# Kernel tuning notes

Hardware: AMD Instinct MI355X
Metric: run time of the kernel (lower is better)

## Reference

```python
import jax, jax.numpy as jnp
import numpy as np

STROKE_SIZE = 200000
WORD_SIZE = 100000
EMB_DIM = 128
BATCH = 16384
MAX_STROKE_LEN = 20
N_SAMPLE = 5


def setup_inputs() -> dict:
    key = jax.random.key(0)
    k1, k2, k3, k4, k5 = jax.random.split(key, 5)
    initrange = 0.5 / EMB_DIM
    u_emb = jax.random.uniform(k1, (STROKE_SIZE, EMB_DIM), jnp.float32,
                               minval=-initrange, maxval=initrange)
    # original inits v to zeros (degenerate loss); use small random values so
    # the score/loss path is numerically non-trivial for kernel testing.
    v_emb = jax.random.normal(k2, (WORD_SIZE, EMB_DIM), jnp.float32) * initrange
    pos_u = jax.random.randint(k3, (BATCH, MAX_STROKE_LEN), 0, STROKE_SIZE)
    pos_v = jax.random.randint(k4, (BATCH, MAX_STROKE_LEN), 0, WORD_SIZE)
    neg_v = jax.random.randint(k5, (BATCH, N_SAMPLE, MAX_STROKE_LEN), 0, WORD_SIZE)
    return {
        "max_stroke_len": MAX_STROKE_LEN,
        "n_sample": N_SAMPLE,
        "pos_u": pos_u,
        "pos_v": pos_v,
        "neg_v": neg_v,
        "u_emb": u_emb,
        "v_emb": v_emb,
    }


def reference(max_stroke_len, n_sample, pos_u, pos_v, neg_v, u_emb, v_emb):
    # gather + mean-pool n-gram embeddings: [B, L, D] -> [B, D]
    emb_u = u_emb[pos_u].mean(axis=1)
    emb_v = v_emb[pos_v].mean(axis=1)
    # positive score: log sigmoid(u . v)  (== sigmoid().log() in original)
    log_target = jax.nn.log_sigmoid(jnp.sum(emb_u * emb_v, axis=1))  # [B]
    # negative samples: [B, S, L, D] -> mean over L -> negate -> [B, S, D]
    neg_emb_v = -v_emb[neg_v].mean(axis=2)
    # bmm(neg_emb_v, emb_u): [B, S]
    neg_scores = jnp.einsum('bsd,bd->bs', neg_emb_v, emb_u)
    sum_log_sampled = jax.nn.log_sigmoid(neg_scores).sum(axis=1)  # [B]
    loss = log_target + sum_log_sampled
    return -loss.mean()
```

## Files before the change

kernel.cpp:

```cpp
#include <hip/hip_runtime.h>
#include <hip/hip_fp16.h>


constexpr int BATCH  = 16384;
constexpr int LEN    = 20;
constexpr int NS     = 5;
constexpr int DIM    = 128;
constexpr int WPB    = 4;
constexpr int V_ROWS = 100000;

__device__ __forceinline__ float log_sigmoid(float x) {
    return fminf(x, 0.0f) - log1pf(expf(-fabsf(x)));
}

__device__ __forceinline__ void acc4(float4& a, const float4 b) {
    a.x += b.x; a.y += b.y; a.z += b.z; a.w += b.w;
}

__device__ __forceinline__ float4 combine_halves(float4 v) {
    float4 r;
    r.x = v.x + __shfl_xor(v.x, 32, 64);
    r.y = v.y + __shfl_xor(v.y, 32, 64);
    r.z = v.z + __shfl_xor(v.z, 32, 64);
    r.w = v.w + __shfl_xor(v.w, 32, 64);
    return r;
}

__device__ __forceinline__ float dot4(const float4 a, const float4 b) {
    return a.x*b.x + a.y*b.y + a.z*b.z + a.w*b.w;
}

__device__ __forceinline__ float half_reduce(float v) {
    v += __shfl_xor(v, 16, 64);
    v += __shfl_xor(v, 8, 64);
    v += __shfl_xor(v, 4, 64);
    v += __shfl_xor(v, 2, 64);
    v += __shfl_xor(v, 1, 64);
    return v;
}

__device__ __forceinline__ unsigned int enc_e5m2(float v) {
    unsigned short h = __half_as_ushort(__float2half(v));
    return ((unsigned int)h + 0x80u) >> 8;
}
__device__ __forceinline__ float4 dec_e5m2x4(unsigned int w) {
    float4 r;
    r.x = __half2float(__ushort_as_half((unsigned short)((w & 0x000000ffu) << 8)));
    r.y = __half2float(__ushort_as_half((unsigned short)( w & 0x0000ff00u)));
    r.z = __half2float(__ushort_as_half((unsigned short)((w >> 8) & 0x0000ff00u)));
    r.w = __half2float(__ushort_as_half((unsigned short)((w >> 16) & 0x0000ff00u)));
    return r;
}

__global__ __launch_bounds__(256) void sg_pack(
    const float* __restrict__ v_emb, unsigned int* __restrict__ v8)
{
    const size_t i = (size_t)blockIdx.x * blockDim.x + threadIdx.x;
    const size_t n = (size_t)V_ROWS * DIM / 4;
    if (i >= n) return;
    const float4 v = *reinterpret_cast<const float4*>(v_emb + i * 4);
    v8[i] = enc_e5m2(v.x) | (enc_e5m2(v.y) << 8) |
            (enc_e5m2(v.z) << 16) | (enc_e5m2(v.w) << 24);
}

__global__ __launch_bounds__(WPB*64) void sg_u(
    const int* __restrict__ pos_u, const float* __restrict__ u_emb,
    float* __restrict__ eu_out)
{
    const int w    = threadIdx.x >> 6;
    const int b    = blockIdx.x * WPB + w;
    const int t    = threadIdx.x & 63;
    const int half = t >> 5;
    const int q    = t & 31;

    __shared__ int sidx[WPB * LEN];
    if (threadIdx.x < WPB * LEN)
        sidx[threadIdx.x] = pos_u[(size_t)blockIdx.x * WPB * LEN + threadIdx.x];
    __syncthreads();

    float4 su = {0.f, 0.f, 0.f, 0.f};
    #pragma unroll
    for (int k = 0; k < LEN / 2; ++k) {
        const int l = 2 * k + half;
        acc4(su, *(reinterpret_cast<const float4*>(
                       u_emb + (size_t)sidx[w * LEN + l] * DIM) + q));
    }
    const float4 eu = combine_halves(su);
    if (half == 0)
        *reinterpret_cast<float4*>(eu_out + (size_t)b * DIM + q * 4) = eu;
}

__global__ __launch_bounds__(WPB*64) void sg_v8(
    const int* __restrict__ pos_v, const int* __restrict__ neg_v,
    const unsigned int* __restrict__ v8, const float* __restrict__ eu_in,
    float* __restrict__ partials)
{
    const int w    = threadIdx.x >> 6;
    const int b    = blockIdx.x * WPB + w;
    const int t    = threadIdx.x & 63;
    const int half = t >> 5;
    const int q    = t & 31;

    __shared__ int spos[WPB * LEN];
    __shared__ int sneg[WPB * NS * LEN];
    if (threadIdx.x < WPB * LEN)
        spos[threadIdx.x] = pos_v[(size_t)blockIdx.x * WPB * LEN + threadIdx.x];
    for (int i = threadIdx.x; i < WPB * NS * LEN; i += WPB * 64)
        sneg[i] = neg_v[(size_t)blockIdx.x * WPB * NS * LEN + i];
    __syncthreads();

    const float4 eu = *reinterpret_cast<const float4*>(
        eu_in + (size_t)b * DIM + q * 4);

    float4 sv = {0.f, 0.f, 0.f, 0.f};
    float4 sn[NS];
    #pragma unroll
    for (int s = 0; s < NS; ++s) sn[s] = {0.f, 0.f, 0.f, 0.f};

    #pragma unroll
    for (int k = 0; k < LEN / 2; ++k) {
        const int l = 2 * k + half;
        acc4(sv, dec_e5m2x4(v8[(size_t)spos[w * LEN + l] * 32 + q]));
    }
    #pragma unroll
    for (int s = 0; s < NS; ++s) {
        #pragma unroll
        for (int k = 0; k < LEN / 2; ++k) {
            const int l = 2 * k + half;
            acc4(sn[s], dec_e5m2x4(v8[(size_t)sneg[(w * NS + s) * LEN + l] * 32 + q]));
        }
    }

    constexpr float inv_LL = 1.0f / (float(LEN) * float(LEN));

    const float4 ev = combine_halves(sv);
    float loss = log_sigmoid(half_reduce(dot4(eu, ev)) * inv_LL);
    #pragma unroll
    for (int s = 0; s < NS; ++s) {
        const float4 nv = combine_halves(sn[s]);
        loss += log_sigmoid(-half_reduce(dot4(nv, eu)) * inv_LL);
    }

    if (t == 0) partials[b] = loss;
}

__global__ __launch_bounds__(1024) void sg_reduce(
    const float* __restrict__ partials, float* __restrict__ out)
{
    const int t = threadIdx.x;
    float acc = 0.f;
    for (int i = t; i < BATCH; i += 1024) acc += partials[i];
    #pragma unroll
    for (int m = 32; m >= 1; m >>= 1) acc += __shfl_xor(acc, m, 64);
    __shared__ float sh[16];
    if ((t & 63) == 0) sh[t >> 6] = acc;
    __syncthreads();
    if (t == 0) {
        float s = 0.f;
        #pragma unroll
        for (int i = 0; i < 16; ++i) s += sh[i];
        out[0] = -s * (1.0f / float(BATCH));
    }
}

__global__ __launch_bounds__(WPB*64) void sg_v(
    const int* __restrict__ pos_v, const int* __restrict__ neg_v,
    const float* __restrict__ v_emb, const float* __restrict__ eu_in,
    float* __restrict__ partials)
{
    const int w    = threadIdx.x >> 6;
    const int b    = blockIdx.x * WPB + w;
    const int t    = threadIdx.x & 63;
    const int half = t >> 5;
    const int q    = t & 31;

    __shared__ int spos[WPB * LEN];
    __shared__ int sneg[WPB * NS * LEN];
    if (threadIdx.x < WPB * LEN)
        spos[threadIdx.x] = pos_v[(size_t)blockIdx.x * WPB * LEN + threadIdx.x];
    for (int i = threadIdx.x; i < WPB * NS * LEN; i += WPB * 64)
        sneg[i] = neg_v[(size_t)blockIdx.x * WPB * NS * LEN + i];
    __syncthreads();

    const float4 eu = *reinterpret_cast<const float4*>(
        eu_in + (size_t)b * DIM + q * 4);

    float4 sv = {0.f, 0.f, 0.f, 0.f};
    float4 sn[NS];
    #pragma unroll
    for (int s = 0; s < NS; ++s) sn[s] = {0.f, 0.f, 0.f, 0.f};

    #pragma unroll
    for (int k = 0; k < LEN / 2; ++k) {
        const int l = 2 * k + half;
        acc4(sv, *(reinterpret_cast<const float4*>(
                       v_emb + (size_t)spos[w * LEN + l] * DIM) + q));
    }
    #pragma unroll
    for (int s = 0; s < NS; ++s) {
        #pragma unroll
        for (int k = 0; k < LEN / 2; ++k) {
            const int l = 2 * k + half;
            acc4(sn[s], *(reinterpret_cast<const float4*>(
                              v_emb + (size_t)sneg[(w * NS + s) * LEN + l] * DIM) + q));
        }
    }

    constexpr float inv_LL = 1.0f / (float(LEN) * float(LEN));
    const float4 ev = combine_halves(sv);
    float loss = log_sigmoid(half_reduce(dot4(eu, ev)) * inv_LL);
    #pragma unroll
    for (int s = 0; s < NS; ++s) {
        const float4 nv = combine_halves(sn[s]);
        loss += log_sigmoid(-half_reduce(dot4(nv, eu)) * inv_LL);
    }
    if (t == 0) partials[b] = loss;
}

extern "C" void kernel_launch(void* const* d_in, const int* in_sizes, int n_in,
                              void* d_out, int out_size, void* d_ws, size_t ws_size,
                              hipStream_t stream) {
    const int*   pos_u = (const int*)d_in[2];
    const int*   pos_v = (const int*)d_in[3];
    const int*   neg_v = (const int*)d_in[4];
    const float* u_emb = (const float*)d_in[5];
    const float* v_emb = (const float*)d_in[6];
    float*       out   = (float*)d_out;

    const size_t v8_bytes = (size_t)V_ROWS * DIM;
    const size_t eu_bytes = (size_t)BATCH * DIM * sizeof(float);
    const size_t pr_bytes = (size_t)BATCH * sizeof(float);

    if (ws_size >= v8_bytes + eu_bytes + pr_bytes) {
        unsigned int* v8_ws  = (unsigned int*)d_ws;
        float* eu_ws         = (float*)((char*)d_ws + v8_bytes);
        float* partials      = (float*)((char*)d_ws + v8_bytes + eu_bytes);
        const int pack_elems = V_ROWS * DIM / 4;
        sg_pack<<<(pack_elems + 255) / 256, 256, 0, stream>>>(v_emb, v8_ws);
        sg_u<<<BATCH / WPB, WPB * 64, 0, stream>>>(pos_u, u_emb, eu_ws);
        sg_v8<<<BATCH / WPB, WPB * 64, 0, stream>>>(pos_v, neg_v, v8_ws, eu_ws, partials);
        sg_reduce<<<1, 1024, 0, stream>>>(partials, out);
    } else if (ws_size >= eu_bytes + pr_bytes) {
        float* eu_ws    = (float*)d_ws;
        float* partials = (float*)((char*)d_ws + eu_bytes);
        sg_u<<<BATCH / WPB, WPB * 64, 0, stream>>>(pos_u, u_emb, eu_ws);
        sg_v<<<BATCH / WPB, WPB * 64, 0, stream>>>(pos_v, neg_v, v_emb, eu_ws, partials);
        sg_reduce<<<1, 1024, 0, stream>>>(partials, out);
    }
}
```

Baseline: 253.7 us.

## Reorder loss by v row via counting sort and per-row dot scatter

Replaces the per-batch gather of v rows with a counting sort of all positive and negative v occurrences by row (histogram, three-pass scan, atomic scatter). Each row of v_emb is then read once and dotted against the pooled u vectors of every batch entry that references it, with results atomically accumulated per (batch, sample). u_emb is also packed to an 8-bit e5m2 format before pooling, and the pooled u is stored in that format. The aim is to cut redundant random v-row traffic, at the cost of many extra launches, atomics, a large workspace and lower precision on the u side.

```diff
diff --git a/kernel.cpp b/kernel.cpp
--- a/kernel.cpp
+++ b/kernel.cpp
@@ -6,17 +6,21 @@
 constexpr int LEN    = 20;
 constexpr int NS     = 5;
 constexpr int DIM    = 128;
-constexpr int WPB    = 4;
+constexpr int U_ROWS = 200000;
 constexpr int V_ROWS = 100000;
+constexpr int POS_OCC = BATCH * LEN;
+constexpr int OCC     = BATCH * LEN * (1 + NS);
+constexpr int NCHUNK  = (V_ROWS + 1023) / 1024;
 
 __device__ __forceinline__ float log_sigmoid(float x) {
     return fminf(x, 0.0f) - log1pf(expf(-fabsf(x)));
 }
-
 __device__ __forceinline__ void acc4(float4& a, const float4 b) {
     a.x += b.x; a.y += b.y; a.z += b.z; a.w += b.w;
 }
-
+__device__ __forceinline__ float dot4(const float4 a, const float4 b) {
+    return a.x*b.x + a.y*b.y + a.z*b.z + a.w*b.w;
+}
 __device__ __forceinline__ float4 combine_halves(float4 v) {
     float4 r;
     r.x = v.x + __shfl_xor(v.x, 32, 64);
@@ -25,11 +29,6 @@
     r.w = v.w + __shfl_xor(v.w, 32, 64);
     return r;
 }
-
-__device__ __forceinline__ float dot4(const float4 a, const float4 b) {
-    return a.x*b.x + a.y*b.y + a.z*b.z + a.w*b.w;
-}
-
 __device__ __forceinline__ float half_reduce(float v) {
     v += __shfl_xor(v, 16, 64);
     v += __shfl_xor(v, 8, 64);
@@ -43,6 +42,10 @@
     unsigned short h = __half_as_ushort(__float2half(v));
     return ((unsigned int)h + 0x80u) >> 8;
 }
+__device__ __forceinline__ unsigned int enc_e5m2x4(float4 v) {
+    return enc_e5m2(v.x) | (enc_e5m2(v.y) << 8) |
+           (enc_e5m2(v.z) << 16) | (enc_e5m2(v.w) << 24);
+}
 __device__ __forceinline__ float4 dec_e5m2x4(unsigned int w) {
     float4 r;
     r.x = __half2float(__ushort_as_half((unsigned short)((w & 0x000000ffu) << 8)));
@@ -52,96 +55,170 @@
     return r;
 }
 
-__global__ __launch_bounds__(256) void sg_pack(
-    const float* __restrict__ v_emb, unsigned int* __restrict__ v8)
-{
-    const size_t i = (size_t)blockIdx.x * blockDim.x + threadIdx.x;
-    const size_t n = (size_t)V_ROWS * DIM / 4;
+__global__ __launch_bounds__(256) void sg_pack_u(
+    const float* __restrict__ u_emb, unsigned int* __restrict__ u8)
+{
+    const size_t i = (size_t)blockIdx.x * 256 + threadIdx.x;
+    const size_t n = (size_t)U_ROWS * DIM / 4;
     if (i >= n) return;
-    const float4 v = *reinterpret_cast<const float4*>(v_emb + i * 4);
-    v8[i] = enc_e5m2(v.x) | (enc_e5m2(v.y) << 8) |
-            (enc_e5m2(v.z) << 16) | (enc_e5m2(v.w) << 24);
-}
-
-__global__ __launch_bounds__(WPB*64) void sg_u(
-    const int* __restrict__ pos_u, const float* __restrict__ u_emb,
-    float* __restrict__ eu_out)
+    u8[i] = enc_e5m2x4(*reinterpret_cast<const float4*>(u_emb + i * 4));
+}
+
+__global__ __launch_bounds__(256) void sg_u8(
+    const int* __restrict__ pos_u, const unsigned int* __restrict__ u8,
+    unsigned int* __restrict__ eu8)
 {
     const int w    = threadIdx.x >> 6;
-    const int b    = blockIdx.x * WPB + w;
+    const int b    = blockIdx.x * 4 + w;
     const int t    = threadIdx.x & 63;
     const int half = t >> 5;
     const int q    = t & 31;
 
-    __shared__ int sidx[WPB * LEN];
-    if (threadIdx.x < WPB * LEN)
-        sidx[threadIdx.x] = pos_u[(size_t)blockIdx.x * WPB * LEN + threadIdx.x];
+    __shared__ int sidx[4 * LEN];
+    if (threadIdx.x < 4 * LEN)
+        sidx[threadIdx.x] = pos_u[(size_t)blockIdx.x * 4 * LEN + threadIdx.x];
     __syncthreads();
 
     float4 su = {0.f, 0.f, 0.f, 0.f};
     #pragma unroll
     for (int k = 0; k < LEN / 2; ++k) {
         const int l = 2 * k + half;
-        acc4(su, *(reinterpret_cast<const float4*>(
-                       u_emb + (size_t)sidx[w * LEN + l] * DIM) + q));
+        acc4(su, dec_e5m2x4(u8[(size_t)sidx[w * LEN + l] * 32 + q]));
     }
     const float4 eu = combine_halves(su);
-    if (half == 0)
-        *reinterpret_cast<float4*>(eu_out + (size_t)b * DIM + q * 4) = eu;
-}
-
-__global__ __launch_bounds__(WPB*64) void sg_v8(
+    if (half == 0) eu8[(size_t)b * 32 + q] = enc_e5m2x4(eu);
+}
+
+__global__ __launch_bounds__(256) void sg_hist(
     const int* __restrict__ pos_v, const int* __restrict__ neg_v,
-    const unsigned int* __restrict__ v8, const float* __restrict__ eu_in,
-    float* __restrict__ partials)
-{
-    const int w    = threadIdx.x >> 6;
-    const int b    = blockIdx.x * WPB + w;
-    const int t    = threadIdx.x & 63;
-    const int half = t >> 5;
-    const int q    = t & 31;
-
-    __shared__ int spos[WPB * LEN];
-    __shared__ int sneg[WPB * NS * LEN];
-    if (threadIdx.x < WPB * LEN)
-        spos[threadIdx.x] = pos_v[(size_t)blockIdx.x * WPB * LEN + threadIdx.x];
-    for (int i = threadIdx.x; i < WPB * NS * LEN; i += WPB * 64)
-        sneg[i] = neg_v[(size_t)blockIdx.x * WPB * NS * LEN + i];
-    __syncthreads();
-
-    const float4 eu = *reinterpret_cast<const float4*>(
-        eu_in + (size_t)b * DIM + q * 4);
-
-    float4 sv = {0.f, 0.f, 0.f, 0.f};
-    float4 sn[NS];
-    #pragma unroll
-    for (int s = 0; s < NS; ++s) sn[s] = {0.f, 0.f, 0.f, 0.f};
-
-    #pragma unroll
-    for (int k = 0; k < LEN / 2; ++k) {
-        const int l = 2 * k + half;
-        acc4(sv, dec_e5m2x4(v8[(size_t)spos[w * LEN + l] * 32 + q]));
-    }
-    #pragma unroll
-    for (int s = 0; s < NS; ++s) {
+    int* __restrict__ counts)
+{
+    const int stride = gridDim.x * 256;
+    for (int e = blockIdx.x * 256 + threadIdx.x; e < POS_OCC; e += stride)
+        atomicAdd(&counts[pos_v[e]], 1);
+    for (int e = blockIdx.x * 256 + threadIdx.x; e < OCC - POS_OCC; e += stride)
+        atomicAdd(&counts[neg_v[e]], 1);
+}
+
+__global__ __launch_bounds__(1024) void sg_scanA(
+    const int* __restrict__ counts, int* __restrict__ offsets,
+    int* __restrict__ totals)
+{
+    __shared__ int wsum[16];
+    const int tid  = threadIdx.x;
+    const int gid  = blockIdx.x * 1024 + tid;
+    const int lane = tid & 63, w = tid >> 6;
+    const int v = (gid < V_ROWS) ? counts[gid] : 0;
+    int x = v;
+    #pragma unroll
+    for (int d = 1; d < 64; d <<= 1) {
+        int y = __shfl_up(x, d, 64);
+        if (lane >= d) x += y;
+    }
+    if (lane == 63) wsum[w] = x;
+    __syncthreads();
+    if (w == 0) {
+        int s = (lane < 16) ? wsum[lane] : 0;
         #pragma unroll
-        for (int k = 0; k < LEN / 2; ++k) {
-            const int l = 2 * k + half;
-            acc4(sn[s], dec_e5m2x4(v8[(size_t)sneg[(w * NS + s) * LEN + l] * 32 + q]));
+        for (int d = 1; d < 16; d <<= 1) {
+            int y = __shfl_up(s, d, 64);
+            if (lane >= d) s += y;
         }
-    }
-
+        if (lane < 16) wsum[lane] = s;
+    }
+    __syncthreads();
+    const int base = (w > 0) ? wsum[w - 1] : 0;
+    if (gid < V_ROWS) offsets[gid] = base + (x - v);
+    if (tid == 0) totals[blockIdx.x] = wsum[15];
+}
+
+__global__ __launch_bounds__(128) void sg_scanB(int* __restrict__ totals)
+{
+    __shared__ int wsum[2];
+    const int tid = threadIdx.x, lane = tid & 63, w = tid >> 6;
+    const int v = (tid < NCHUNK) ? totals[tid] : 0;
+    int x = v;
+    #pragma unroll
+    for (int d = 1; d < 64; d <<= 1) {
+        int y = __shfl_up(x, d, 64);
+        if (lane >= d) x += y;
+    }
+    if (lane == 63) wsum[w] = x;
+    __syncthreads();
+    const int base = (w == 1) ? wsum[0] : 0;
+    if (tid < NCHUNK) totals[tid] = base + (x - v);
+}
+
+__global__ __launch_bounds__(1024) void sg_scanC(
+    int* __restrict__ offsets, const int* __restrict__ totals)
+{
+    const int gid = blockIdx.x * 1024 + threadIdx.x;
+    if (gid < V_ROWS) offsets[gid] += totals[blockIdx.x];
+    if (gid == 0) offsets[V_ROWS] = OCC;
+}
+
+__global__ __launch_bounds__(256) void sg_scatter(
+    const int* __restrict__ pos_v, const int* __restrict__ neg_v,
+    int* __restrict__ cursor, unsigned int* __restrict__ sorted)
+{
+    const int stride = gridDim.x * 256;
+    for (int e = blockIdx.x * 256 + threadIdx.x; e < OCC; e += stride) {
+        int r, payload;
+        if (e < POS_OCC) {
+            r = pos_v[e];
+            payload = ((e / LEN) << 3) | 5;
+        } else {
+            const int e2 = e - POS_OCC;
+            r = neg_v[e2];
+            const int b = e2 / (NS * LEN);
+            const int s = (e2 / LEN) % NS;
+            payload = (b << 3) | s;
+        }
+        const int p = atomicAdd(&cursor[r], 1);
+        sorted[p] = (unsigned int)payload;
+    }
+}
+
+__global__ __launch_bounds__(256) void sg_dot(
+    const float* __restrict__ v_emb, const unsigned int* __restrict__ eu8,
+    const int* __restrict__ offsets, const unsigned int* __restrict__ sorted,
+    float* __restrict__ c)
+{
+    const int row = (blockIdx.x * 256 + threadIdx.x) >> 6;
+    if (row >= V_ROWS) return;
+    const int t = threadIdx.x & 63, half = t >> 5, q = t & 31;
+    const int off0 = offsets[row], off1 = offsets[row + 1];
+    if (off0 == off1) return;
+
+    const float4 vr = *(reinterpret_cast<const float4*>(
+                            v_emb + (size_t)row * DIM) + q);
+
+    for (int i = off0; i < off1; i += 2) {
+        const int j = i + half;
+        float val = 0.f;
+        unsigned int payload = 0;
+        if (j < off1) {
+            payload = sorted[j];
+            const unsigned int b = payload >> 3;
+            val = dot4(vr, dec_e5m2x4(eu8[(size_t)b * 32 + q]));
+        }
+        val = half_reduce(val);
+        if ((t & 31) == 0 && j < off1)
+            atomicAdd(&c[(payload >> 3) * 8 + (payload & 7u)], val);
+    }
+}
+
+__global__ __launch_bounds__(256) void sg_final(
+    const float* __restrict__ c, float* __restrict__ partials)
+{
+    const int b = blockIdx.x * 256 + threadIdx.x;
+    if (b >= BATCH) return;
     constexpr float inv_LL = 1.0f / (float(LEN) * float(LEN));
-
-    const float4 ev = combine_halves(sv);
-    float loss = log_sigmoid(half_reduce(dot4(eu, ev)) * inv_LL);
-    #pragma unroll
-    for (int s = 0; s < NS; ++s) {
-        const float4 nv = combine_halves(sn[s]);
-        loss += log_sigmoid(-half_reduce(dot4(nv, eu)) * inv_LL);
-    }
-
-    if (t == 0) partials[b] = loss;
+    float loss = log_sigmoid(c[b * 8 + 5] * inv_LL);
+    #pragma unroll
+    for (int s = 0; s < NS; ++s)
+        loss += log_sigmoid(-c[b * 8 + s] * inv_LL);
+    partials[b] = loss;
 }
 
 __global__ __launch_bounds__(1024) void sg_reduce(
@@ -163,33 +240,49 @@
     }
 }
 
-__global__ __launch_bounds__(WPB*64) void sg_v(
+__global__ __launch_bounds__(256) void sg_u_f32(
+    const int* __restrict__ pos_u, const float* __restrict__ u_emb,
+    float* __restrict__ eu_out)
+{
+    const int w = threadIdx.x >> 6;
+    const int b = blockIdx.x * 4 + w;
+    const int t = threadIdx.x & 63, half = t >> 5, q = t & 31;
+    __shared__ int sidx[4 * LEN];
+    if (threadIdx.x < 4 * LEN)
+        sidx[threadIdx.x] = pos_u[(size_t)blockIdx.x * 4 * LEN + threadIdx.x];
+    __syncthreads();
+    float4 su = {0, 0, 0, 0};
+    #pragma unroll
+    for (int k = 0; k < LEN / 2; ++k) {
+        const int l = 2 * k + half;
+        acc4(su, *(reinterpret_cast<const float4*>(
+                       u_emb + (size_t)sidx[w * LEN + l] * DIM) + q));
+    }
+    const float4 eu = combine_halves(su);
+    if (half == 0)
+        *reinterpret_cast<float4*>(eu_out + (size_t)b * DIM + q * 4) = eu;
+}
+
+__global__ __launch_bounds__(256) void sg_v_f32(
     const int* __restrict__ pos_v, const int* __restrict__ neg_v,
     const float* __restrict__ v_emb, const float* __restrict__ eu_in,
     float* __restrict__ partials)
 {
-    const int w    = threadIdx.x >> 6;
-    const int b    = blockIdx.x * WPB + w;
-    const int t    = threadIdx.x & 63;
-    const int half = t >> 5;
-    const int q    = t & 31;
-
-    __shared__ int spos[WPB * LEN];
-    __shared__ int sneg[WPB * NS * LEN];
-    if (threadIdx.x < WPB * LEN)
-        spos[threadIdx.x] = pos_v[(size_t)blockIdx.x * WPB * LEN + threadIdx.x];
-    for (int i = threadIdx.x; i < WPB * NS * LEN; i += WPB * 64)
-        sneg[i] = neg_v[(size_t)blockIdx.x * WPB * NS * LEN + i];
-    __syncthreads();
-
-    const float4 eu = *reinterpret_cast<const float4*>(
-        eu_in + (size_t)b * DIM + q * 4);
-
-    float4 sv = {0.f, 0.f, 0.f, 0.f};
+    const int w = threadIdx.x >> 6;
+    const int b = blockIdx.x * 4 + w;
+    const int t = threadIdx.x & 63, half = t >> 5, q = t & 31;
+    __shared__ int spos[4 * LEN];
+    __shared__ int sneg[4 * NS * LEN];
+    if (threadIdx.x < 4 * LEN)
+        spos[threadIdx.x] = pos_v[(size_t)blockIdx.x * 4 * LEN + threadIdx.x];
+    for (int i = threadIdx.x; i < 4 * NS * LEN; i += 256)
+        sneg[i] = neg_v[(size_t)blockIdx.x * 4 * NS * LEN + i];
+    __syncthreads();
+    const float4 eu = *reinterpret_cast<const float4*>(eu_in + (size_t)b * DIM + q * 4);
+    float4 sv = {0, 0, 0, 0};
     float4 sn[NS];
     #pragma unroll
-    for (int s = 0; s < NS; ++s) sn[s] = {0.f, 0.f, 0.f, 0.f};
-
+    for (int s = 0; s < NS; ++s) sn[s] = {0, 0, 0, 0};
     #pragma unroll
     for (int k = 0; k < LEN / 2; ++k) {
         const int l = 2 * k + half;
@@ -205,7 +298,6 @@
                               v_emb + (size_t)sneg[(w * NS + s) * LEN + l] * DIM) + q));
         }
     }
-
     constexpr float inv_LL = 1.0f / (float(LEN) * float(LEN));
     const float4 ev = combine_halves(sv);
     float loss = log_sigmoid(half_reduce(dot4(eu, ev)) * inv_LL);
@@ -227,24 +319,52 @@
     const float* v_emb = (const float*)d_in[6];
     float*       out   = (float*)d_out;
 
-    const size_t v8_bytes = (size_t)V_ROWS * DIM;
-    const size_t eu_bytes = (size_t)BATCH * DIM * sizeof(float);
-    const size_t pr_bytes = (size_t)BATCH * sizeof(float);
-
-    if (ws_size >= v8_bytes + eu_bytes + pr_bytes) {
-        unsigned int* v8_ws  = (unsigned int*)d_ws;
-        float* eu_ws         = (float*)((char*)d_ws + v8_bytes);
-        float* partials      = (float*)((char*)d_ws + v8_bytes + eu_bytes);
-        const int pack_elems = V_ROWS * DIM / 4;
-        sg_pack<<<(pack_elems + 255) / 256, 256, 0, stream>>>(v_emb, v8_ws);
-        sg_u<<<BATCH / WPB, WPB * 64, 0, stream>>>(pos_u, u_emb, eu_ws);
-        sg_v8<<<BATCH / WPB, WPB * 64, 0, stream>>>(pos_v, neg_v, v8_ws, eu_ws, partials);
+    const size_t u8_off      = 0;
+    const size_t eu8_off     = 25600000;
+    const size_t counts_off  = 27697152;
+    const size_t c_off       = 28097280;
+    const size_t offsets_off = 28621568;
+    const size_t totals_off  = 29021952;
+    const size_t cursor_off  = 29022464;
+    const size_t sorted_off  = 29422592;
+    const size_t part_off    = 37286912;
+    const size_t need        = part_off + 65536;
+
+    char* ws = (char*)d_ws;
+
+    if (ws_size >= need) {
+        unsigned int* u8      = (unsigned int*)(ws + u8_off);
+        unsigned int* eu8     = (unsigned int*)(ws + eu8_off);
+        int*          counts  = (int*)(ws + counts_off);
+        float*        c       = (float*)(ws + c_off);
+        int*          offsets = (int*)(ws + offsets_off);
+        int*          totals  = (int*)(ws + totals_off);
+        int*          cursor  = (int*)(ws + cursor_off);
+        unsigned int* sorted  = (unsigned int*)(ws + sorted_off);
+        float*        partials= (float*)(ws + part_off);
+
+        hipMemsetAsync(ws + counts_off, 0, (c_off - counts_off) + 524288, stream);
+
+        sg_pack_u<<<(U_ROWS * DIM / 4 + 255) / 256, 256, 0, stream>>>(u_emb, u8);
+        sg_u8<<<BATCH / 4, 256, 0, stream>>>(pos_u, u8, eu8);
+
+        sg_hist<<<1024, 256, 0, stream>>>(pos_v, neg_v, counts);
+        sg_scanA<<<NCHUNK, 1024, 0, stream>>>(counts, offsets, totals);
+        sg_scanB<<<1, 128, 0, stream>>>(totals);
+        sg_scanC<<<NCHUNK, 1024, 0, stream>>>(offsets, totals);
+        hipMemcpyAsync(cursor, offsets, (size_t)V_ROWS * sizeof(int),
+                       hipMemcpyDeviceToDevice, stream);
+        sg_scatter<<<2048, 256, 0, stream>>>(pos_v, neg_v, cursor, sorted);
+
+        sg_dot<<<(V_ROWS + 3) / 4, 256, 0, stream>>>(v_emb, eu8, offsets, sorted, c);
+
+        sg_final<<<(BATCH + 255) / 256, 256, 0, stream>>>(c, partials);
         sg_reduce<<<1, 1024, 0, stream>>>(partials, out);
-    } else if (ws_size >= eu_bytes + pr_bytes) {
+    } else {
         float* eu_ws    = (float*)d_ws;
-        float* partials = (float*)((char*)d_ws + eu_bytes);
-        sg_u<<<BATCH / WPB, WPB * 64, 0, stream>>>(pos_u, u_emb, eu_ws);
-        sg_v<<<BATCH / WPB, WPB * 64, 0, stream>>>(pos_v, neg_v, v_emb, eu_ws, partials);
+        float* partials = (float*)((char*)d_ws + (size_t)BATCH * DIM * sizeof(float));
+        sg_u_f32<<<BATCH / 4, 256, 0, stream>>>(pos_u, u_emb, eu_ws);
+        sg_v_f32<<<BATCH / 4, 256, 0, stream>>>(pos_v, neg_v, v_emb, eu_ws, partials);
         sg_reduce<<<1, 1024, 0, stream>>>(partials, out);
     }
 }
```

New measurement: 610.5 us. +140.6%, slower.
